# Performance work log

Hardware: AMD Instinct MI355X
Metric: run time of the kernel (lower is better)

Reference implementation:

```python
import jax, jax.numpy as jnp
import numpy as np

N_NODES = 100000
N_EDGES = 1250000
NUM_SKILLS = 100000
HID = 64


def _sage(h, src, dst, Wl, bl, Wr, n):
    # SAGEConv (PyG defaults): out = lin_l(mean_{j in N(i)} h_j) + lin_r(h_i)
    msgs = h[src]                                        # [E, d] gather
    agg = jax.ops.segment_sum(msgs, dst, num_segments=n)  # [N, d]
    cnt = jax.ops.segment_sum(jnp.ones((src.shape[0],), h.dtype), dst, num_segments=n)
    mean = agg / jnp.maximum(cnt, 1.0)[:, None]
    return mean @ Wl + bl + h @ Wr


def _prelu(v, a):
    return jnp.where(v >= 0, v, a * v)


def setup_inputs() -> dict:
    key = jax.random.key(0)
    ks = jax.random.split(key, 12)
    s = 1.0 / np.sqrt(HID)
    inp = {
        "x": jax.random.randint(ks[0], (N_NODES,), 0, NUM_SKILLS),
        "edge_index": jax.random.randint(ks[1], (2, N_EDGES), 0, N_NODES),
        "edge_weight": jax.random.uniform(ks[2], (N_EDGES,), jnp.float32),
        "emb": jax.random.normal(ks[3], (NUM_SKILLS, HID), jnp.float32),
        "Wl1": jax.random.uniform(ks[4], (HID, HID), jnp.float32, -s, s),
        "bl1": jnp.zeros((HID,), jnp.float32),
        "Wr1": jax.random.uniform(ks[5], (HID, HID), jnp.float32, -s, s),
        "a1": jnp.float32(0.25),
        "Wl2": jax.random.uniform(ks[6], (HID, HID), jnp.float32, -s, s),
        "bl2": jnp.zeros((HID,), jnp.float32),
        "Wr2": jax.random.uniform(ks[7], (HID, HID), jnp.float32, -s, s),
        "a2": jnp.float32(0.25),
        "Wout": jax.random.uniform(ks[8], (HID, HID), jnp.float32, -s, s),
        "bout": jnp.zeros((HID,), jnp.float32),
    }
    return inp


def reference(x, edge_index, edge_weight, emb, Wl1, bl1, Wr1, a1,
              Wl2, bl2, Wr2, a2, Wout, bout):
    src, dst = edge_index[0], edge_index[1]
    n = x.shape[0]
    h0 = emb[x]                                           # [N, d] embedding lookup
    h1 = _prelu(_sage(h0, src, dst, Wl1, bl1, Wr1, n), a1)  # dropout = identity (eval)
    h2 = _prelu(_sage(h1, src, dst, Wl2, bl2, Wr2, n), a2)
    return h2 @ Wout + bout
```

## Files before the change

### kernel.cpp

```cpp
#include <hip/hip_runtime.h>
#include <hip/hip_bf16.h>

#define N_NODES 100000
#define N_EDGES 1250000
#define HID 64
#define LDSS 72
#define NB 196
#define NBLOCK 128
#define EMB_BLOCKS 6250

typedef __bf16 bf16x8 __attribute__((ext_vector_type(8)));
typedef float  f32x4  __attribute__((ext_vector_type(4)));

__device__ __forceinline__ float bflo(uint u) {
    union { unsigned int i; float f; } v; v.i = u << 16; return v.f;
}
__device__ __forceinline__ float bfhi(uint u) {
    union { unsigned int i; float f; } v; v.i = u & 0xFFFF0000u; return v.f;
}
__device__ __forceinline__ ushort f2bf(float f) {
    union { float f; unsigned int i; } v; v.f = f;
    unsigned int x = v.i;
    return (ushort)((x + 0x7fffu + ((x >> 16) & 1u)) >> 16);
}

__global__ __launch_bounds__(256) void hist_k(const int* __restrict__ dst,
                                              int* __restrict__ gh) {
    __shared__ int hist[NB];
    const int tid = threadIdx.x;
    for (int i = tid; i < NB; i += 256) hist[i] = 0;
    __syncthreads();
    const int4* d4 = (const int4*)dst;
    for (int e = blockIdx.x * 256 + tid; e < N_EDGES / 4; e += NBLOCK * 256) {
        int4 v = d4[e];
        atomicAdd(&hist[v.x >> 9], 1);
        atomicAdd(&hist[v.y >> 9], 1);
        atomicAdd(&hist[v.z >> 9], 1);
        atomicAdd(&hist[v.w >> 9], 1);
    }
    __syncthreads();
    for (int i = tid; i < NB; i += 256) gh[blockIdx.x * NB + i] = hist[i];
}

__global__ __launch_bounds__(256) void work2(const int* __restrict__ x,
                                             const float* __restrict__ emb,
                                             ushort* __restrict__ h0,
                                             const int* __restrict__ src,
                                             const int* __restrict__ dst,
                                             const int* __restrict__ gh,
                                             int* __restrict__ bstart,
                                             uint* __restrict__ ebuf,
                                             const float* __restrict__ Wl1,
                                             const float* __restrict__ Wr1,
                                             const float* __restrict__ Wl2,
                                             const float* __restrict__ Wr2,
                                             const float* __restrict__ Wout,
                                             ushort* __restrict__ wbf) {
    const int b = blockIdx.x;
    const int tid = threadIdx.x;
    if (b < NBLOCK) {
        __shared__ int base[NB];
        __shared__ int run[NB];
        __shared__ int wsum[4];
        const int lane = tid & 63, wave = tid >> 6;
        int myTot = 0, myPre = 0;
        if (tid < NB) {
#pragma unroll 8
            for (int bb = 0; bb < NBLOCK; ++bb) {
                int c = gh[bb * NB + tid];
                if (bb == b) myPre = myTot;
                myTot += c;
            }
        }
        int x2 = myTot;
#pragma unroll
        for (int d = 1; d < 64; d <<= 1) {
            int y = __shfl_up(x2, d, 64);
            if (lane >= d) x2 += y;
        }
        if (lane == 63) wsum[wave] = x2;
        __syncthreads();
        if (wave == 0) {
            int s = (lane < 4) ? wsum[lane] : 0;
#pragma unroll
            for (int d = 1; d < 4; d <<= 1) {
                int y = __shfl_up(s, d, 64);
                if (lane >= d) s += y;
            }
            if (lane < 4) wsum[lane] = s;
        }
        __syncthreads();
        int waveoff = (wave == 0) ? 0 : wsum[wave - 1];
        int excl = waveoff + (x2 - myTot);
        if (tid < NB) {
            base[tid] = excl + myPre;
            run[tid] = 0;
            if (b == 0) bstart[tid] = excl;
        }
        if (b == 0 && tid == 0) bstart[NB] = N_EDGES;
        __syncthreads();
        const int4* s4 = (const int4*)src;
        const int4* d4 = (const int4*)dst;
        for (int e = b * 256 + tid; e < N_EDGES / 4; e += NBLOCK * 256) {
            int4 dv = d4[e];
            int4 sv = s4[e];
            int b0 = dv.x >> 9;
            int r0 = atomicAdd(&run[b0], 1);
            ebuf[base[b0] + r0] = ((uint)(dv.x & 511) << 17) | (uint)sv.x;
            int b1 = dv.y >> 9;
            int r1 = atomicAdd(&run[b1], 1);
            ebuf[base[b1] + r1] = ((uint)(dv.y & 511) << 17) | (uint)sv.y;
            int b2 = dv.z >> 9;
            int r2 = atomicAdd(&run[b2], 1);
            ebuf[base[b2] + r2] = ((uint)(dv.z & 511) << 17) | (uint)sv.z;
            int b3 = dv.w >> 9;
            int r3 = atomicAdd(&run[b3], 1);
            ebuf[base[b3] + r3] = ((uint)(dv.w & 511) << 17) | (uint)sv.w;
        }
    } else if (b < NBLOCK + EMB_BLOCKS) {
        int t = (b - NBLOCK) * 256 + tid;
        int row = t >> 4, c = t & 15;
        int idx = x[row];
        float4 v = ((const float4*)(emb + (size_t)idx * HID))[c];
        ushort4 w;
        w.x = f2bf(v.x); w.y = f2bf(v.y); w.z = f2bf(v.z); w.w = f2bf(v.w);
        ((ushort4*)(h0 + (size_t)row * HID))[c] = w;
    } else {
        const int wb = b - NBLOCK - EMB_BLOCKS;
        const float* W = (wb == 0) ? Wl1 : (wb == 1) ? Wr1 :
                         (wb == 2) ? Wl2 : (wb == 3) ? Wr2 : Wout;
        ushort* o = wbf + wb * 4096;
        for (int idx = tid; idx < 4096; idx += 256) {
            int k = idx >> 6, n = idx & 63;
            o[n * 64 + k] = f2bf(W[idx]);
        }
    }
}

__global__ __launch_bounds__(256) void p4_csr(const uint* __restrict__ ebuf,
                                              const int* __restrict__ bstart,
                                              int* __restrict__ rowptr,
                                              int* __restrict__ csr_src) {
    __shared__ int hist[512], hoff[512], run[512];
    __shared__ int wsum[4];
    const int v = blockIdx.x;
    const int tid = threadIdx.x, lane = tid & 63, wave = tid >> 6;
    const int node0 = v << 9;
    const int nn = min(512, N_NODES - node0);
    const int beg = bstart[v], end = bstart[v + 1];

    for (int i = tid; i < 512; i += 256) { hist[i] = 0; run[i] = 0; }
    __syncthreads();
    for (int e = beg + tid; e < end; e += 256)
        atomicAdd(&hist[ebuf[e] >> 17], 1);
    __syncthreads();
    int h0 = hist[2 * tid], h1 = hist[2 * tid + 1];
    int s = h0 + h1;
    int x = s;
#pragma unroll
    for (int d = 1; d < 64; d <<= 1) {
        int y = __shfl_up(x, d, 64);
        if (lane >= d) x += y;
    }
    if (lane == 63) wsum[wave] = x;
    __syncthreads();
    if (wave == 0) {
        int s2 = (lane < 4) ? wsum[lane] : 0;
#pragma unroll
        for (int d = 1; d < 4; d <<= 1) {
            int y = __shfl_up(s2, d, 64);
            if (lane >= d) s2 += y;
        }
        if (lane < 4) wsum[lane] = s2;
    }
    __syncthreads();
    int waveoff = (wave == 0) ? 0 : wsum[wave - 1];
    int excl = waveoff + (x - s);
    hoff[2 * tid] = excl;
    hoff[2 * tid + 1] = excl + h0;
    __syncthreads();
    for (int j = tid; j < nn; j += 256) rowptr[node0 + j] = beg + hoff[j];
    if (v == NB - 1 && tid == 0) rowptr[N_NODES] = N_EDGES;
    for (int e = beg + tid; e < end; e += 256) {
        uint p = ebuf[e];
        int dl = p >> 17;
        int r = atomicAdd(&run[dl], 1);
        csr_src[beg + hoff[dl] + r] = (int)(p & 0x1FFFFu);
    }
}

#define ACCUM(wa, wb)                                                      \
    a0 += bflo(wa.x); a1 += bfhi(wa.x); a2 += bflo(wa.y); a3 += bfhi(wa.y); \
    a4 += bflo(wa.z); a5 += bfhi(wa.z); a6 += bflo(wa.w); a7 += bfhi(wa.w); \
    a8 += bflo(wb.x); a9 += bfhi(wb.x); a10 += bflo(wb.y); a11 += bfhi(wb.y); \
    a12 += bflo(wb.z); a13 += bfhi(wb.z); a14 += bflo(wb.w); a15 += bfhi(wb.w);

#define GATHER(j)                                                          \
    const uint4* p##j = (const uint4*)&hin[(size_t)s##j * HID + q * 16];   \
    uint4 A##j = p##j[0], B##j = p##j[1];

#define SHXOR(OFF)                                                          \
    a0 += __shfl_xor(a0, OFF, 64);   a1 += __shfl_xor(a1, OFF, 64);         \
    a2 += __shfl_xor(a2, OFF, 64);   a3 += __shfl_xor(a3, OFF, 64);         \
    a4 += __shfl_xor(a4, OFF, 64);   a5 += __shfl_xor(a5, OFF, 64);         \
    a6 += __shfl_xor(a6, OFF, 64);   a7 += __shfl_xor(a7, OFF, 64);         \
    a8 += __shfl_xor(a8, OFF, 64);   a9 += __shfl_xor(a9, OFF, 64);         \
    a10 += __shfl_xor(a10, OFF, 64); a11 += __shfl_xor(a11, OFF, 64);       \
    a12 += __shfl_xor(a12, OFF, 64); a13 += __shfl_xor(a13, OFF, 64);       \
    a14 += __shfl_xor(a14, OFF, 64); a15 += __shfl_xor(a15, OFF, 64);

template <bool OUTPROJ>
__global__ __launch_bounds__(256, 4) void layer_fused(
    const int* __restrict__ rowptr, const int* __restrict__ csr_src,
    const ushort* __restrict__ hin,
    const ushort* __restrict__ wl_bf, const float* __restrict__ bl,
    const ushort* __restrict__ wr_bf, const float* __restrict__ alpha_p,
    const ushort* __restrict__ wo_bf, const float* __restrict__ bo,
    void* __restrict__ out_p) {
    __shared__ __align__(16) ushort sA[16][LDSS];

    const int tid = threadIdx.x;
    const int row0 = blockIdx.x * 16;
    const int wave = tid >> 6, lane = tid & 63;

    const int nl = tid >> 4, hh = (tid >> 2) & 3, q = tid & 3;
    {
        const int node = row0 + nl;
        const int beg = rowptr[node], end = rowptr[node + 1];
        const int d = end - beg;
        const int hbeg = beg + ((d * hh) >> 2);
        const int hend = beg + ((d * (hh + 1)) >> 2);
        float a0 = 0.f, a1 = 0.f, a2 = 0.f, a3 = 0.f;
        float a4 = 0.f, a5 = 0.f, a6 = 0.f, a7 = 0.f;
        float a8 = 0.f, a9 = 0.f, a10 = 0.f, a11 = 0.f;
        float a12 = 0.f, a13 = 0.f, a14 = 0.f, a15 = 0.f;
        int i = hbeg;
        for (; i + 8 <= hend; i += 8) {
            int s0 = csr_src[i + 0], s1 = csr_src[i + 1];
            int s2 = csr_src[i + 2], s3 = csr_src[i + 3];
            int s4 = csr_src[i + 4], s5 = csr_src[i + 5];
            int s6 = csr_src[i + 6], s7 = csr_src[i + 7];
            GATHER(0) GATHER(1) GATHER(2) GATHER(3)
            GATHER(4) GATHER(5) GATHER(6) GATHER(7)
            ACCUM(A0, B0) ACCUM(A1, B1) ACCUM(A2, B2) ACCUM(A3, B3)
            ACCUM(A4, B4) ACCUM(A5, B5) ACCUM(A6, B6) ACCUM(A7, B7)
        }
        if (i < hend) {
            const int e1 = hend - 1;
            int s0 = csr_src[i + 0];
            int s1 = csr_src[(i + 1 <= e1) ? i + 1 : e1];
            int s2 = csr_src[(i + 2 <= e1) ? i + 2 : e1];
            int s3 = csr_src[(i + 3 <= e1) ? i + 3 : e1];
            int s4 = csr_src[(i + 4 <= e1) ? i + 4 : e1];
            int s5 = csr_src[(i + 5 <= e1) ? i + 5 : e1];
            int s6 = csr_src[(i + 6 <= e1) ? i + 6 : e1];
            int s7 = csr_src[(i + 7 <= e1) ? i + 7 : e1];
            GATHER(0) GATHER(1) GATHER(2) GATHER(3)
            GATHER(4) GATHER(5) GATHER(6) GATHER(7)
            const uint4 z = {0, 0, 0, 0};
            if (i + 1 > e1) { A1 = z; B1 = z; }
            if (i + 2 > e1) { A2 = z; B2 = z; }
            if (i + 3 > e1) { A3 = z; B3 = z; }
            if (i + 4 > e1) { A4 = z; B4 = z; }
            if (i + 5 > e1) { A5 = z; B5 = z; }
            if (i + 6 > e1) { A6 = z; B6 = z; }
            if (i + 7 > e1) { A7 = z; B7 = z; }
            ACCUM(A0, B0) ACCUM(A1, B1) ACCUM(A2, B2) ACCUM(A3, B3)
            ACCUM(A4, B4) ACCUM(A5, B5) ACCUM(A6, B6) ACCUM(A7, B7)
        }
        SHXOR(4)
        SHXOR(8)
        if (hh == 0) {
            float inv = (d > 0) ? 1.0f / (float)d : 0.f;
            uint4 o0, o1;
            o0.x = (uint)f2bf(a0 * inv)  | ((uint)f2bf(a1 * inv) << 16);
            o0.y = (uint)f2bf(a2 * inv)  | ((uint)f2bf(a3 * inv) << 16);
            o0.z = (uint)f2bf(a4 * inv)  | ((uint)f2bf(a5 * inv) << 16);
            o0.w = (uint)f2bf(a6 * inv)  | ((uint)f2bf(a7 * inv) << 16);
            o1.x = (uint)f2bf(a8 * inv)  | ((uint)f2bf(a9 * inv) << 16);
            o1.y = (uint)f2bf(a10 * inv) | ((uint)f2bf(a11 * inv) << 16);
            o1.z = (uint)f2bf(a12 * inv) | ((uint)f2bf(a13 * inv) << 16);
            o1.w = (uint)f2bf(a14 * inv) | ((uint)f2bf(a15 * inv) << 16);
            *(uint4*)&sA[nl][q * 16] = o0;
            *(uint4*)&sA[nl][q * 16 + 8] = o1;
        }
    }
    __syncthreads();
    if (wave >= 1) return;

    const int quad = lane >> 4, lr = lane & 15;
    const int grow = row0 + lr;
    const float alpha = alpha_p[0];

    bf16x8 hf[2], af[2];
#pragma unroll
    for (int ks = 0; ks < 2; ++ks) {
        int k0 = ks * 32 + quad * 8;
        uint4 hv = *(const uint4*)&hin[(size_t)grow * HID + k0];
        hf[ks] = __builtin_bit_cast(bf16x8, hv);
        uint4 av = *(const uint4*)&sA[lr][k0];
        af[ks] = __builtin_bit_cast(bf16x8, av);
    }

    f32x4 acc[4];
#pragma unroll
    for (int nt = 0; nt < 4; ++nt) {
        f32x4 a = {0.f, 0.f, 0.f, 0.f};
#pragma unroll
        for (int ks = 0; ks < 2; ++ks) {
            int k0 = ks * 32 + quad * 8;
            bf16x8 wr = *(const bf16x8*)&wr_bf[(nt * 16 + lr) * 64 + k0];
            a = __builtin_amdgcn_mfma_f32_16x16x32_bf16(hf[ks], wr, a, 0, 0, 0);
            bf16x8 wl = *(const bf16x8*)&wl_bf[(nt * 16 + lr) * 64 + k0];
            a = __builtin_amdgcn_mfma_f32_16x16x32_bf16(af[ks], wl, a, 0, 0, 0);
        }
        acc[nt] = a;
    }

    if constexpr (!OUTPROJ) {
#pragma unroll
        for (int nt = 0; nt < 4; ++nt) {
            int col = nt * 16 + lr;
            float bias = bl[col];
#pragma unroll
            for (int r = 0; r < 4; ++r) {
                int row = quad * 4 + r;
                float v = acc[nt][r] + bias;
                v = (v >= 0.f) ? v : alpha * v;
                sA[row][col] = f2bf(v);
            }
        }
        ushort* outp = (ushort*)out_p;
        const int lrow = lane >> 3, lch = lane & 7;
#pragma unroll
        for (int pass = 0; pass < 2; ++pass) {
            int row = pass * 8 + lrow;
            int gg2 = row0 + row;
            uint4 v4 = *(const uint4*)&sA[row][lch * 8];
            *(uint4*)&outp[(size_t)gg2 * HID + lch * 8] = v4;
        }
    } else {
#pragma unroll
        for (int nt = 0; nt < 4; ++nt) {
            int col = nt * 16 + lr;
            float bias = bl[col];
#pragma unroll
            for (int r = 0; r < 4; ++r) {
                int row = quad * 4 + r;
                float v = acc[nt][r] + bias;
                v = (v >= 0.f) ? v : alpha * v;
                sA[row][col] = f2bf(v);
            }
        }
        bf16x8 h2f[2];
#pragma unroll
        for (int ks = 0; ks < 2; ++ks) {
            int k0 = ks * 32 + quad * 8;
            uint4 hv = *(const uint4*)&sA[lr][k0];
            h2f[ks] = __builtin_bit_cast(bf16x8, hv);
        }
        f32x4 acc2[4];
#pragma unroll
        for (int nt = 0; nt < 4; ++nt) {
            f32x4 a = {0.f, 0.f, 0.f, 0.f};
#pragma unroll
            for (int ks = 0; ks < 2; ++ks) {
                int k0 = ks * 32 + quad * 8;
                bf16x8 wo = *(const bf16x8*)&wo_bf[(nt * 16 + lr) * 64 + k0];
                a = __builtin_amdgcn_mfma_f32_16x16x32_bf16(h2f[ks], wo, a, 0, 0, 0);
            }
            acc2[nt] = a;
        }
        float* outp = (float*)out_p;
#pragma unroll
        for (int nt = 0; nt < 4; ++nt) {
            int col = nt * 16 + lr;
            float bias = bo[col];
#pragma unroll
            for (int r = 0; r < 4; ++r) {
                int row = quad * 4 + r;
                int gg2 = row0 + row;
                outp[(size_t)gg2 * HID + col] = acc2[nt][r] + bias;
            }
        }
    }
}

extern "C" void kernel_launch(void* const* d_in, const int* in_sizes, int n_in,
                              void* d_out, int out_size, void* d_ws, size_t ws_size,
                              hipStream_t stream) {
    const int*   x    = (const int*)d_in[0];
    const int*   src  = (const int*)d_in[1];
    const int*   dst  = src + N_EDGES;
    const float* emb  = (const float*)d_in[3];
    const float* Wl1  = (const float*)d_in[4];
    const float* bl1  = (const float*)d_in[5];
    const float* Wr1  = (const float*)d_in[6];
    const float* a1   = (const float*)d_in[7];
    const float* Wl2  = (const float*)d_in[8];
    const float* bl2  = (const float*)d_in[9];
    const float* Wr2  = (const float*)d_in[10];
    const float* a2   = (const float*)d_in[11];
    const float* Wout = (const float*)d_in[12];
    const float* bout = (const float*)d_in[13];

    char* ws = (char*)d_ws;
    int*    gh      = (int*)ws;
    int*    bstart  = (int*)(ws + 101248);
    int*    rowptr  = (int*)(ws + 102080);
    ushort* wbf     = (ushort*)(ws + 502144);
    uint*   ebuf    = (uint*)(ws + 543104);
    int*    csr_src = (int*)(ws + 5543104);
    ushort* h0      = (ushort*)(ws + 10543104);
    ushort* h1      = (ushort*)(ws + 23343104);

    ushort* wl1b  = wbf;
    ushort* wr1b  = wbf + 4096;
    ushort* wl2b  = wbf + 8192;
    ushort* wr2b  = wbf + 12288;
    ushort* woutb = wbf + 16384;

    const int layer_blocks = N_NODES / 16;

    hist_k<<<NBLOCK, 256, 0, stream>>>(dst, gh);
    work2<<<NBLOCK + EMB_BLOCKS + 5, 256, 0, stream>>>(
        x, emb, h0, src, dst, gh, bstart, ebuf, Wl1, Wr1, Wl2, Wr2, Wout, wbf);
    p4_csr<<<NB, 256, 0, stream>>>(ebuf, bstart, rowptr, csr_src);

    layer_fused<false><<<layer_blocks, 256, 0, stream>>>(
        rowptr, csr_src, h0, wl1b, bl1, wr1b, a1, wr1b, bl1, h1);
    layer_fused<true><<<layer_blocks, 256, 0, stream>>>(
        rowptr, csr_src, h1, wl2b, bl2, wr2b, a2, woutb, bout, d_out);
}
```

Measured before the change: 217.8 us.

## Spread embedding lookup blocks across the three CSR-build kernels

The embedding gather and bf16 conversion, which used to run only inside the scatter kernel, is now split into three chunks. Each chunk is appended as extra blocks to the histogram, scatter and CSR-finalize kernels. These small CSR kernels use few blocks and leave the GPU underoccupied, so the idle compute units can do embedding work alongside them. The risk is extra scheduling interference and a longer tail in the phases that were short.

```diff
diff --git a/kernel.cpp b/kernel.cpp
--- a/kernel.cpp
+++ b/kernel.cpp
@@ -8,6 +8,9 @@
 #define NB 196
 #define NBLOCK 128
 #define EMB_BLOCKS 6250
+#define EMB_A 2000
+#define EMB_B 2000
+#define EMB_C 2250
 
 typedef __bf16 bf16x8 __attribute__((ext_vector_type(8)));
 typedef float  f32x4  __attribute__((ext_vector_type(4)));
@@ -24,38 +27,59 @@
     return (ushort)((x + 0x7fffu + ((x >> 16) & 1u)) >> 16);
 }
 
-__global__ __launch_bounds__(256) void hist_k(const int* __restrict__ dst,
-                                              int* __restrict__ gh) {
-    __shared__ int hist[NB];
+__device__ __forceinline__ void embed_rows(int eb, int tid,
+                                           const int* __restrict__ x,
+                                           const float* __restrict__ emb,
+                                           ushort* __restrict__ h0) {
+    int t = eb * 256 + tid;
+    int row = t >> 4, c = t & 15;
+    int idx = x[row];
+    float4 v = ((const float4*)(emb + (size_t)idx * HID))[c];
+    ushort4 w;
+    w.x = f2bf(v.x); w.y = f2bf(v.y); w.z = f2bf(v.z); w.w = f2bf(v.w);
+    ((ushort4*)(h0 + (size_t)row * HID))[c] = w;
+}
+
+__global__ __launch_bounds__(256) void k1_hist_embed(const int* __restrict__ dst,
+                                                     int* __restrict__ gh,
+                                                     const int* __restrict__ x,
+                                                     const float* __restrict__ emb,
+                                                     ushort* __restrict__ h0) {
+    const int b = blockIdx.x;
     const int tid = threadIdx.x;
-    for (int i = tid; i < NB; i += 256) hist[i] = 0;
-    __syncthreads();
-    const int4* d4 = (const int4*)dst;
-    for (int e = blockIdx.x * 256 + tid; e < N_EDGES / 4; e += NBLOCK * 256) {
-        int4 v = d4[e];
-        atomicAdd(&hist[v.x >> 9], 1);
-        atomicAdd(&hist[v.y >> 9], 1);
-        atomicAdd(&hist[v.z >> 9], 1);
-        atomicAdd(&hist[v.w >> 9], 1);
-    }
-    __syncthreads();
-    for (int i = tid; i < NB; i += 256) gh[blockIdx.x * NB + i] = hist[i];
-}
-
-__global__ __launch_bounds__(256) void work2(const int* __restrict__ x,
-                                             const float* __restrict__ emb,
-                                             ushort* __restrict__ h0,
-                                             const int* __restrict__ src,
-                                             const int* __restrict__ dst,
-                                             const int* __restrict__ gh,
-                                             int* __restrict__ bstart,
-                                             uint* __restrict__ ebuf,
-                                             const float* __restrict__ Wl1,
-                                             const float* __restrict__ Wr1,
-                                             const float* __restrict__ Wl2,
-                                             const float* __restrict__ Wr2,
-                                             const float* __restrict__ Wout,
-                                             ushort* __restrict__ wbf) {
+    if (b < NBLOCK) {
+        __shared__ int hist[NB];
+        for (int i = tid; i < NB; i += 256) hist[i] = 0;
+        __syncthreads();
+        const int4* d4 = (const int4*)dst;
+        for (int e = b * 256 + tid; e < N_EDGES / 4; e += NBLOCK * 256) {
+            int4 v = d4[e];
+            atomicAdd(&hist[v.x >> 9], 1);
+            atomicAdd(&hist[v.y >> 9], 1);
+            atomicAdd(&hist[v.z >> 9], 1);
+            atomicAdd(&hist[v.w >> 9], 1);
+        }
+        __syncthreads();
+        for (int i = tid; i < NB; i += 256) gh[b * NB + i] = hist[i];
+    } else {
+        embed_rows(b - NBLOCK, tid, x, emb, h0);
+    }
+}
+
+__global__ __launch_bounds__(256) void k2_p3_embed(const int* __restrict__ src,
+                                                   const int* __restrict__ dst,
+                                                   const int* __restrict__ gh,
+                                                   int* __restrict__ bstart,
+                                                   uint* __restrict__ ebuf,
+                                                   const int* __restrict__ x,
+                                                   const float* __restrict__ emb,
+                                                   ushort* __restrict__ h0,
+                                                   const float* __restrict__ Wl1,
+                                                   const float* __restrict__ Wr1,
+                                                   const float* __restrict__ Wl2,
+                                                   const float* __restrict__ Wr2,
+                                                   const float* __restrict__ Wout,
+                                                   ushort* __restrict__ wbf) {
     const int b = blockIdx.x;
     const int tid = threadIdx.x;
     if (b < NBLOCK) {
@@ -117,16 +141,10 @@
             int r3 = atomicAdd(&run[b3], 1);
             ebuf[base[b3] + r3] = ((uint)(dv.w & 511) << 17) | (uint)sv.w;
         }
-    } else if (b < NBLOCK + EMB_BLOCKS) {
-        int t = (b - NBLOCK) * 256 + tid;
-        int row = t >> 4, c = t & 15;
-        int idx = x[row];
-        float4 v = ((const float4*)(emb + (size_t)idx * HID))[c];
-        ushort4 w;
-        w.x = f2bf(v.x); w.y = f2bf(v.y); w.z = f2bf(v.z); w.w = f2bf(v.w);
-        ((ushort4*)(h0 + (size_t)row * HID))[c] = w;
+    } else if (b < NBLOCK + EMB_B) {
+        embed_rows(EMB_A + (b - NBLOCK), tid, x, emb, h0);
     } else {
-        const int wb = b - NBLOCK - EMB_BLOCKS;
+        const int wb = b - NBLOCK - EMB_B;
         const float* W = (wb == 0) ? Wl1 : (wb == 1) ? Wr1 :
                          (wb == 2) ? Wl2 : (wb == 3) ? Wr2 : Wout;
         ushort* o = wbf + wb * 4096;
@@ -137,14 +155,23 @@
     }
 }
 
-__global__ __launch_bounds__(256) void p4_csr(const uint* __restrict__ ebuf,
-                                              const int* __restrict__ bstart,
-                                              int* __restrict__ rowptr,
-                                              int* __restrict__ csr_src) {
+__global__ __launch_bounds__(256) void k3_p4_embed(const uint* __restrict__ ebuf,
+                                                   const int* __restrict__ bstart,
+                                                   int* __restrict__ rowptr,
+                                                   int* __restrict__ csr_src,
+                                                   const int* __restrict__ x,
+                                                   const float* __restrict__ emb,
+                                                   ushort* __restrict__ h0) {
+    const int b = blockIdx.x;
+    const int tid = threadIdx.x;
+    if (b >= NB) {
+        embed_rows(EMB_A + EMB_B + (b - NB), tid, x, emb, h0);
+        return;
+    }
     __shared__ int hist[512], hoff[512], run[512];
     __shared__ int wsum[4];
-    const int v = blockIdx.x;
-    const int tid = threadIdx.x, lane = tid & 63, wave = tid >> 6;
+    const int v = b;
+    const int lane = tid & 63, wave = tid >> 6;
     const int node0 = v << 9;
     const int nn = min(512, N_NODES - node0);
     const int beg = bstart[v], end = bstart[v + 1];
@@ -154,15 +181,15 @@
     for (int e = beg + tid; e < end; e += 256)
         atomicAdd(&hist[ebuf[e] >> 17], 1);
     __syncthreads();
-    int h0 = hist[2 * tid], h1 = hist[2 * tid + 1];
-    int s = h0 + h1;
-    int x = s;
+    int h0c = hist[2 * tid], h1c = hist[2 * tid + 1];
+    int s = h0c + h1c;
+    int x2 = s;
 #pragma unroll
     for (int d = 1; d < 64; d <<= 1) {
-        int y = __shfl_up(x, d, 64);
-        if (lane >= d) x += y;
-    }
-    if (lane == 63) wsum[wave] = x;
+        int y = __shfl_up(x2, d, 64);
+        if (lane >= d) x2 += y;
+    }
+    if (lane == 63) wsum[wave] = x2;
     __syncthreads();
     if (wave == 0) {
         int s2 = (lane < 4) ? wsum[lane] : 0;
@@ -175,9 +202,9 @@
     }
     __syncthreads();
     int waveoff = (wave == 0) ? 0 : wsum[wave - 1];
-    int excl = waveoff + (x - s);
+    int excl = waveoff + (x2 - s);
     hoff[2 * tid] = excl;
-    hoff[2 * tid + 1] = excl + h0;
+    hoff[2 * tid + 1] = excl + h0c;
     __syncthreads();
     for (int j = tid; j < nn; j += 256) rowptr[node0 + j] = beg + hoff[j];
     if (v == NB - 1 && tid == 0) rowptr[N_NODES] = N_EDGES;
@@ -422,10 +449,11 @@
 
     const int layer_blocks = N_NODES / 16;
 
-    hist_k<<<NBLOCK, 256, 0, stream>>>(dst, gh);
-    work2<<<NBLOCK + EMB_BLOCKS + 5, 256, 0, stream>>>(
-        x, emb, h0, src, dst, gh, bstart, ebuf, Wl1, Wr1, Wl2, Wr2, Wout, wbf);
-    p4_csr<<<NB, 256, 0, stream>>>(ebuf, bstart, rowptr, csr_src);
+    k1_hist_embed<<<NBLOCK + EMB_A, 256, 0, stream>>>(dst, gh, x, emb, h0);
+    k2_p3_embed<<<NBLOCK + EMB_B + 5, 256, 0, stream>>>(
+        src, dst, gh, bstart, ebuf, x, emb, h0, Wl1, Wr1, Wl2, Wr2, Wout, wbf);
+    k3_p4_embed<<<NB + EMB_C, 256, 0, stream>>>(
+        ebuf, bstart, rowptr, csr_src, x, emb, h0);
 
     layer_fused<false><<<layer_blocks, 256, 0, stream>>>(
         rowptr, csr_src, h0, wl1b, bl1, wr1b, a1, wr1b, bl1, h1);
```

Measured after the change: 222.2 us. About the same (+2.0%).
